# Kernel optimization log

Measured on AMD Instinct MI355X. Metric: run time of the kernel, lower is better.

The kernel has to match this reference:

```python
import jax, jax.numpy as jnp
import numpy as np

B, N, D, S, H = 32, 4096, 256, 16, 512
ITERS = 3
EPS = 1e-8
LN_EPS = 1e-5  # torch LayerNorm default


def _ln(x, w, b):
    m = jnp.mean(x, axis=-1, keepdims=True)
    v = jnp.mean(jnp.square(x - m), axis=-1, keepdims=True)
    return (x - m) / jnp.sqrt(v + LN_EPS) * w + b


def setup_inputs() -> dict:
    key = jax.random.key(0)
    ks = jax.random.split(key, 20)
    s = 1.0 / np.sqrt(D)
    return {
        "inputs": jax.random.normal(ks[0], (B, N, D), jnp.float32),
        "token_weight": jax.random.uniform(ks[1], (B, N), jnp.float32),
        "noise": jax.random.normal(ks[2], (B, S, D), jnp.float32),
        "ln_in_w": jnp.ones((D,), jnp.float32), "ln_in_b": jnp.zeros((D,), jnp.float32),
        "ln_s_w": jnp.ones((D,), jnp.float32), "ln_s_b": jnp.zeros((D,), jnp.float32),
        "ln_m_w": jnp.ones((D,), jnp.float32), "ln_m_b": jnp.zeros((D,), jnp.float32),
        "Wk": jax.random.normal(ks[3], (D, D), jnp.float32) * s,
        "Wv": jax.random.normal(ks[4], (D, D), jnp.float32) * s,
        "Wq": jax.random.normal(ks[5], (D, D), jnp.float32) * s,
        "gru_wih": jax.random.normal(ks[6], (3 * D, D), jnp.float32) * s,
        "gru_whh": jax.random.normal(ks[7], (3 * D, D), jnp.float32) * s,
        "gru_bih": jax.random.normal(ks[8], (3 * D,), jnp.float32) * s,
        "gru_bhh": jax.random.normal(ks[9], (3 * D,), jnp.float32) * s,
        "mlp_w1": jax.random.normal(ks[10], (H, D), jnp.float32) * s,
        "mlp_b1": jnp.zeros((H,), jnp.float32),
        "mlp_w2": jax.random.normal(ks[11], (D, H), jnp.float32) * (1.0 / np.sqrt(H)),
        "mlp_b2": jnp.zeros((D,), jnp.float32),
        "slots_mu": jax.random.normal(ks[12], (1, 1, D), jnp.float32) * 0.02,
        "slots_logsigma": jax.random.normal(ks[13], (1, 1, D), jnp.float32) * 0.02,
    }


def _gru(x, h, wih, whh, bih, bhh):
    # torch GRUCell: gates ordered r, z, n
    gi = x @ wih.T + bih  # [BS, 3D]
    gh = h @ whh.T + bhh
    ir, iz, inn = jnp.split(gi, 3, axis=-1)
    hr, hz, hn = jnp.split(gh, 3, axis=-1)
    r = jax.nn.sigmoid(ir + hr)
    z = jax.nn.sigmoid(iz + hz)
    n = jnp.tanh(inn + r * hn)
    return (1.0 - z) * n + z * h


def reference(inputs, token_weight, noise, ln_in_w, ln_in_b, ln_s_w, ln_s_b,
              ln_m_w, ln_m_b, Wk, Wv, Wq, gru_wih, gru_whh, gru_bih, gru_bhh,
              mlp_w1, mlp_b1, mlp_w2, mlp_b2, slots_mu, slots_logsigma):
    tw = jnp.clip(token_weight, 0.0, None)  # [B,N]
    x = _ln(inputs, ln_in_w, ln_in_b)
    k = x @ Wk.T  # [B,N,D]
    v = x @ Wv.T
    sigma = jnp.clip(jnp.exp(slots_logsigma), 1e-6, None)
    slots = slots_mu + sigma * noise  # [B,S,D]
    scale = D ** (-0.5)
    attn = None
    for _ in range(ITERS):
        slots_prev = slots
        q = _ln(slots, ln_s_w, ln_s_b) @ Wq.T  # [B,S,D]
        logits = jnp.einsum('bnd,bmd->bnm', k, q) * scale  # [B,N,S]
        attn = jax.nn.softmax(logits, axis=-1)  # softmax over slots
        attn = attn * tw[:, :, None]
        attn = attn / (jnp.sum(attn, axis=1, keepdims=True) + EPS)  # normalize over tokens
        updates = jnp.einsum('bnm,bnd->bmd', attn, v)  # [B,S,D]
        slots = _gru(updates.reshape(B * S, D), slots_prev.reshape(B * S, D),
                     gru_wih, gru_whh, gru_bih, gru_bhh).reshape(B, S, D)
        h = jax.nn.gelu(_ln(slots, ln_m_w, ln_m_b) @ mlp_w1.T + mlp_b1, approximate=False)
        slots = slots + h @ mlp_w2.T + mlp_b2
    return slots, attn
```

## Files before the change

kernel.cpp:

```cpp
#include <hip/hip_runtime.h>
#include <hip/hip_bf16.h>
#include <math.h>


#define EPS_ 1e-8f
#define LNEPS_ 1e-5f
#define XSW(r) ((((r)&7)<<3) ^ ((((r)>>3)&3)<<4))
#define GLOAD16(gp, lp) __builtin_amdgcn_global_load_lds( \
    (const __attribute__((address_space(1))) unsigned int*)(gp), \
    (__attribute__((address_space(3))) unsigned int*)(lp), 16, 0, 0)

typedef __attribute__((ext_vector_type(8))) short bf16x8;
typedef __attribute__((ext_vector_type(4))) float f32x4;
typedef __attribute__((ext_vector_type(4))) short s16x4;

static __device__ __forceinline__ short f2bf(float f) {
  __hip_bfloat16 h = __float2bfloat16(f);
  union { __hip_bfloat16 h; short s; } u; u.h = h; return u.s;
}
static __device__ __forceinline__ float4 ld4(const float* p){ return *(const float4*)p; }

__global__ __launch_bounds__(256) void k_prep(
    const float* __restrict__ Wq, const float* __restrict__ Wk,
    const float* __restrict__ wih, const float* __restrict__ Wv,
    const float* __restrict__ whh, const float* __restrict__ w1, const float* __restrict__ w2,
    short* __restrict__ MTb, short* __restrict__ Mb, short* __restrict__ whhb,
    short* __restrict__ w1b, short* __restrict__ w2b) {
  int blk = blockIdx.x, t = threadIdx.x;
  if (blk < 64) {
    int e0 = blk*4;
    float a0=0,a1=0,a2=0,a3=0;
    for (int d=0; d<256; d++) {
      float qv = Wq[d*256 + t];
      a0 += qv*Wk[d*256+e0];   a1 += qv*Wk[d*256+e0+1];
      a2 += qv*Wk[d*256+e0+2]; a3 += qv*Wk[d*256+e0+3];
    }
    MTb[(e0  )*256+t]=f2bf(a0); MTb[(e0+1)*256+t]=f2bf(a1);
    MTb[(e0+2)*256+t]=f2bf(a2); MTb[(e0+3)*256+t]=f2bf(a3);
  } else if (blk < 256) {
    int n0 = (blk-64)*4;
    float a0=0,a1=0,a2=0,a3=0;
    for (int d=0; d<256; d++) {
      float vv = Wv[d*256 + t];
      a0 += wih[(n0  )*256+d]*vv; a1 += wih[(n0+1)*256+d]*vv;
      a2 += wih[(n0+2)*256+d]*vv; a3 += wih[(n0+3)*256+d]*vv;
    }
    Mb[(size_t)(n0  )*256+t]=f2bf(a0); Mb[(size_t)(n0+1)*256+t]=f2bf(a1);
    Mb[(size_t)(n0+2)*256+t]=f2bf(a2); Mb[(size_t)(n0+3)*256+t]=f2bf(a3);
  } else {
    int c = (blk-256)*256 + t;
    const float* src; short* dst;
    if (c < 49152) { src=whh; dst=whhb; }
    else if ((c-=49152) < 32768) { src=w1; dst=w1b; }
    else { c-=32768; src=w2; dst=w2b; }
    float4 v = ld4(src + (size_t)c*4);
    short4 o; o.x=f2bf(v.x); o.y=f2bf(v.y); o.z=f2bf(v.z); o.w=f2bf(v.w);
    *(short4*)(dst + (size_t)c*4) = o;
  }
}

__global__ __launch_bounds__(256) void k3a(
    const float* __restrict__ inputs, const float* __restrict__ lnw, const float* __restrict__ lnb,
    short* __restrict__ xbf, const short* __restrict__ qk, const float* __restrict__ twg,
    float* __restrict__ ux_part, float* __restrict__ colsum_part) {
  __shared__ short Xs[64*264];
  __shared__ short QKs[16*264];
  __shared__ short Pt[16*72];
  __shared__ float tws[64];
  __shared__ float cs[16];
  __shared__ float lnwb[512];
  const int t = threadIdx.x;
  const int b = blockIdx.x >> 4;
  const int n0 = (blockIdx.x & 15) * 256;
  const int lane = t & 63, w = t >> 6, l15 = lane & 15, lg = lane >> 4;
  #pragma unroll
  for (int i=0;i<2;i++){
    int cid = t + i*256;
    int row = cid>>5, ck = cid&31;
    *(uint4*)&QKs[row*264 + ck*8] = *(const uint4*)&qk[((size_t)(b*16+row))*256 + ck*8];
  }
  if (t < 64)       *(float4*)&lnwb[t*4]           = ld4(lnw + t*4);
  else if (t < 128) *(float4*)&lnwb[256+(t-64)*4]  = ld4(lnb + (t-64)*4);
  if (t<16) cs[t]=0.f;
  f32x4 uacc[4] = {};
  for (int g=0; g<4; ++g) {
    __syncthreads();
    const size_t rowbase = (size_t)b*4096 + n0 + g*64;
    {
      const float* ing = inputs + rowbase*256;
      const int r = t>>2, c = t&3;
      float4 vv[16];
      #pragma unroll
      for (int k=0;k<16;k++) vv[k] = ld4(ing + r*256 + (c+4*k)*4);
      float s=0.f, sq=0.f;
      #pragma unroll
      for (int k=0;k<16;k++){
        s  += vv[k].x+vv[k].y+vv[k].z+vv[k].w;
        sq += vv[k].x*vv[k].x+vv[k].y*vv[k].y+vv[k].z*vv[k].z+vv[k].w*vv[k].w;
      }
      s += __shfl_xor(s,1);  s += __shfl_xor(s,2);
      sq += __shfl_xor(sq,1); sq += __shfl_xor(sq,2);
      float mean = s*(1.f/256.f);
      float rstd = rsqrtf(sq*(1.f/256.f) - mean*mean + LNEPS_);
      short* xw = xbf + rowbase*256;
      const int sw = XSW(r);
      #pragma unroll
      for (int k=0;k<16;k++){
        int d0 = (c+4*k)*4;
        float4 wv = *(float4*)&lnwb[d0];
        float4 bv = *(float4*)&lnwb[256+d0];
        s16x4 pk;
        pk[0]=f2bf((vv[k].x-mean)*rstd*wv.x+bv.x);
        pk[1]=f2bf((vv[k].y-mean)*rstd*wv.y+bv.y);
        pk[2]=f2bf((vv[k].z-mean)*rstd*wv.z+bv.z);
        pk[3]=f2bf((vv[k].w-mean)*rstd*wv.w+bv.w);
        *(s16x4*)&Xs[r*264 + d0] = pk;
        *(s16x4*)&xw[r*256 + (d0 ^ sw)] = pk;
      }
    }
    if (t<64) tws[t] = fmaxf(twg[rowbase + t], 0.f);
    __syncthreads();
    f32x4 acc = {0.f,0.f,0.f,0.f};
    #pragma unroll
    for (int kk=0;kk<8;kk++){
      bf16x8 af  = *(const bf16x8*)&Xs[(w*16+l15)*264 + kk*32 + lg*8];
      bf16x8 bfr = *(const bf16x8*)&QKs[l15*264 + kk*32 + lg*8];
      acc = __builtin_amdgcn_mfma_f32_16x16x32_bf16(af, bfr, acc, 0,0,0);
    }
    float a4[4];
    #pragma unroll
    for (int q=0;q<4;q++){
      float v = acc[q]*0.0625f;
      float m = v;
      #pragma unroll
      for (int d=1; d<16; d<<=1) m = fmaxf(m, __shfl_xor(m, d, 16));
      float e = __expf(v-m);
      float se = e;
      #pragma unroll
      for (int d=1; d<16; d<<=1) se += __shfl_xor(se, d, 16);
      int row = w*16 + lg*4 + q;
      a4[q] = (e/se)*tws[row];
    }
    float psum = a4[0]+a4[1]+a4[2]+a4[3];
    psum += __shfl_xor(psum, 16);
    psum += __shfl_xor(psum, 32);
    if (lane<16) atomicAdd(&cs[l15], psum);
    s16x4 pk; pk[0]=f2bf(a4[0]); pk[1]=f2bf(a4[1]); pk[2]=f2bf(a4[2]); pk[3]=f2bf(a4[3]);
    *(s16x4*)&Pt[l15*72 + w*16 + lg*4] = pk;
    __syncthreads();
    #pragma unroll
    for (int kk=0;kk<2;kk++){
      bf16x8 a2 = *(const bf16x8*)&Pt[l15*72 + kk*32 + lg*8];
      #pragma unroll
      for (int tt=0;tt<4;tt++){
        int col = w*64 + tt*16 + l15;
        int rbv = kk*32 + lg*8;
        bf16x8 b2;
        #pragma unroll
        for (int j=0;j<8;j++) b2[j] = Xs[(rbv+j)*264 + col];
        uacc[tt] = __builtin_amdgcn_mfma_f32_16x16x32_bf16(a2, b2, uacc[tt], 0,0,0);
      }
    }
  }
  __syncthreads();
  if (t<16) colsum_part[blockIdx.x*16 + t] = cs[t];
  #pragma unroll
  for (int tt=0;tt<4;tt++){
    #pragma unroll
    for (int q=0;q<4;q++)
      ux_part[(size_t)blockIdx.x*4096 + (lg*4+q)*256 + w*64 + tt*16 + l15] = uacc[tt][q];
  }
}

template<int WATTN>
__global__ __launch_bounds__(256, 2) void k3w(
    const short* __restrict__ xbf, const short* __restrict__ qk,
    const float* __restrict__ twg, float* __restrict__ ux_part,
    float* __restrict__ colsum_part, float* __restrict__ attn_un) {
  __shared__ __align__(16) short XsAll[4][32*256];
  __shared__ __align__(16) short PtAll[4][16*40];
  __shared__ __align__(16) short QKs[16*264];
  __shared__ float csAll[4][16];
  const int t = threadIdx.x;
  const int lane = t & 63, w = t >> 6;
  const int l15 = lane & 15, lg = lane >> 4;
  const int b = blockIdx.x >> 4;
  const size_t wrow0 = (size_t)b*4096 + (blockIdx.x & 15)*256 + w*64;
  short* xs = &XsAll[w][0];
  short* pt = &PtAll[w][0];
  {
    const short* src = xbf + wrow0*256 + lane*8;
    #pragma unroll
    for (int j=0;j<16;j++) GLOAD16(src + j*512, xs + j*512);
  }
  #pragma unroll
  for (int i=0;i<2;i++){
    int cid = t + i*256;
    int row = cid>>5, ck = cid&31;
    *(uint4*)&QKs[row*264 + ck*8] = *(const uint4*)&qk[((size_t)(b*16+row))*256 + ck*8];
  }
  __syncthreads();
  f32x4 acc[16] = {};
  float cs_acc = 0.f;
  for (int tl=0; tl<2; ++tl){
    asm volatile("s_waitcnt vmcnt(0)" ::: "memory");
    const size_t rowb = wrow0 + tl*32;
    #pragma unroll
    for (int sub=0; sub<2; ++sub){
      const int ra = sub*16 + l15, sa = XSW(ra);
      f32x4 a1 = {0.f,0.f,0.f,0.f};
      #pragma unroll
      for (int kk=0;kk<8;kk++){
        bf16x8 af  = *(const bf16x8*)&xs[ra*256 + ((kk*32+lg*8) ^ sa)];
        bf16x8 bfr = *(const bf16x8*)&QKs[l15*264 + kk*32 + lg*8];
        a1 = __builtin_amdgcn_mfma_f32_16x16x32_bf16(af, bfr, a1, 0,0,0);
      }
      float a4[4];
      #pragma unroll
      for (int q=0;q<4;q++){
        float v = a1[q]*0.0625f;
        float m = v;
        #pragma unroll
        for (int d=1; d<16; d<<=1) m = fmaxf(m, __shfl_xor(m, d, 16));
        float e = __expf(v-m);
        float se = e;
        #pragma unroll
        for (int d=1; d<16; d<<=1) se += __shfl_xor(se, d, 16);
        int rloc = sub*16 + lg*4 + q;
        float tw = fmaxf(twg[rowb + rloc], 0.f);
        float a = (e/se)*tw;
        a4[q] = a;
        if (WATTN) attn_un[(rowb + rloc)*16 + l15] = a;
      }
      float psum = a4[0]+a4[1]+a4[2]+a4[3];
      psum += __shfl_xor(psum, 16);
      psum += __shfl_xor(psum, 32);
      cs_acc += psum;
      s16x4 pk; pk[0]=f2bf(a4[0]); pk[1]=f2bf(a4[1]); pk[2]=f2bf(a4[2]); pk[3]=f2bf(a4[3]);
      *(s16x4*)&pt[l15*40 + sub*16 + lg*4] = pk;
    }
    {
      bf16x8 pa = *(const bf16x8*)&pt[l15*40 + lg*8];
      #pragma unroll
      for (int et=0; et<16; ++et){
        bf16x8 b2;
        #pragma unroll
        for (int j=0;j<8;j++){
          int r2 = lg*8 + j;
          b2[j] = xs[r2*256 + ((et*16+l15) ^ XSW(r2))];
        }
        acc[et] = __builtin_amdgcn_mfma_f32_16x16x32_bf16(pa, b2, acc[et], 0,0,0);
      }
    }
    if (tl==0){
      const short* src = xbf + (wrow0+32)*256 + lane*8;
      #pragma unroll
      for (int j=0;j<16;j++) GLOAD16(src + j*512, xs + j*512);
    }
  }
  float* xf = (float*)xs;
  #pragma unroll
  for (int et=0; et<16; ++et)
    #pragma unroll
    for (int q=0;q<4;q++)
      xf[(lg*4+q)*256 + et*16 + l15] = acc[et][q];
  if (lane<16) csAll[w][lane] = cs_acc;
  __syncthreads();
  float* up = ux_part + (size_t)blockIdx.x*4096;
  const float4* X0 = (const float4*)&XsAll[0][0];
  const float4* X1 = (const float4*)&XsAll[1][0];
  const float4* X2 = (const float4*)&XsAll[2][0];
  const float4* X3 = (const float4*)&XsAll[3][0];
  #pragma unroll
  for (int i=0;i<4;i++){
    int idx = t + i*256;
    float4 v0=X0[idx], v1=X1[idx], v2=X2[idx], v3=X3[idx];
    float4 o; o.x=v0.x+v1.x+v2.x+v3.x; o.y=v0.y+v1.y+v2.y+v3.y;
    o.z=v0.z+v1.z+v2.z+v3.z; o.w=v0.w+v1.w+v2.w+v3.w;
    *(float4*)&up[idx*4] = o;
  }
  if (t<16) colsum_part[blockIdx.x*16+t] = csAll[0][t]+csAll[1][t]+csAll[2][t]+csAll[3][t];
}

__global__ __launch_bounds__(256) void k_reduce(const float* __restrict__ uxp,
    const float* __restrict__ csp, short* __restrict__ uxr, float* __restrict__ csr) {
  int r = blockIdx.x;
  int b = r>>4, s = r&15;
  int t = threadIdx.x;
  float cs = 0.f;
  #pragma unroll
  for (int k=0;k<16;k++) cs += csp[((b<<4)+k)*16 + s];
  float u = 0.f;
  #pragma unroll
  for (int k=0;k<16;k++) u += uxp[(size_t)((b<<4)+k)*4096 + s*256 + t];
  uxr[(size_t)r*256+t] = f2bf(u/(cs+EPS_));
  if (t==0) csr[r] = cs;
}

__global__ __launch_bounds__(256) void k_gigh(
    const short* __restrict__ uxr, const short* __restrict__ slotsb,
    const short* __restrict__ Mb, const short* __restrict__ whhb,
    const float* __restrict__ bih, const float* __restrict__ bhh,
    float* __restrict__ gig) {
  __shared__ short As[64*40];
  __shared__ short Ws[64*40];
  const int t=threadIdx.x, bn=blockIdx.x, bm=blockIdx.y;
  const short* A; const short* W; const float* bias; int wo;
  if (bn<12) { A=uxr;    W=Mb   + (size_t)bn*64*256;      bias=bih; wo=bn*64; }
  else       { A=slotsb; W=whhb + (size_t)(bn-12)*64*256; bias=bhh; wo=(bn-12)*64; }
  const int w=t>>6, lane=t&63, l15=lane&15, lg=lane>>4;
  f32x4 acc[4]={};
  for (int k0=0;k0<256;k0+=32){
    __syncthreads();
    *(uint4*)&As[(t>>2)*40+(t&3)*8] = *(const uint4*)&A[(size_t)(bm*64+(t>>2))*256 + k0 + (t&3)*8];
    *(uint4*)&Ws[(t>>2)*40+(t&3)*8] = *(const uint4*)&W[(size_t)(t>>2)*256 + k0 + (t&3)*8];
    __syncthreads();
    bf16x8 af = *(const bf16x8*)&As[(w*16+l15)*40+lg*8];
    #pragma unroll
    for (int ct=0;ct<4;ct++){
      bf16x8 bfr = *(const bf16x8*)&Ws[(ct*16+l15)*40+lg*8];
      acc[ct]=__builtin_amdgcn_mfma_f32_16x16x32_bf16(af,bfr,acc[ct],0,0,0);
    }
  }
  #pragma unroll
  for (int ct=0;ct<4;ct++){
    float bv = bias[wo + ct*16 + l15];
    #pragma unroll
    for (int q=0;q<4;q++){
      int row = bm*64 + w*16 + lg*4 + q;
      gig[(size_t)row*1536 + bn*64 + ct*16 + l15] = acc[ct][q] + bv;
    }
  }
}

__global__ __launch_bounds__(256) void k_mlp1(
    const short* __restrict__ lnmb, const short* __restrict__ w1b,
    const float* __restrict__ b1, short* __restrict__ hb) {
  __shared__ short As[64*40];
  __shared__ short Ws[64*40];
  const int t=threadIdx.x, bn=blockIdx.x, bm=blockIdx.y;
  const int w=t>>6, lane=t&63, l15=lane&15, lg=lane>>4;
  f32x4 acc[4]={};
  for (int k0=0;k0<256;k0+=32){
    __syncthreads();
    *(uint4*)&As[(t>>2)*40+(t&3)*8] = *(const uint4*)&lnmb[(size_t)(bm*64+(t>>2))*256 + k0 + (t&3)*8];
    *(uint4*)&Ws[(t>>2)*40+(t&3)*8] = *(const uint4*)&w1b[(size_t)(bn*64+(t>>2))*256 + k0 + (t&3)*8];
    __syncthreads();
    bf16x8 af = *(const bf16x8*)&As[(w*16+l15)*40+lg*8];
    #pragma unroll
    for (int ct=0;ct<4;ct++){
      bf16x8 bfr = *(const bf16x8*)&Ws[(ct*16+l15)*40+lg*8];
      acc[ct]=__builtin_amdgcn_mfma_f32_16x16x32_bf16(af,bfr,acc[ct],0,0,0);
    }
  }
  #pragma unroll
  for (int ct=0;ct<4;ct++){
    float bv = b1[bn*64 + ct*16 + l15];
    #pragma unroll
    for (int q=0;q<4;q++){
      int row = bm*64 + w*16 + lg*4 + q;
      float v = acc[ct][q] + bv;
      v = 0.5f*v*(1.f+erff(v*0.70710678118654752f));
      hb[(size_t)row*512 + bn*64 + ct*16 + l15] = f2bf(v);
    }
  }
}

__global__ __launch_bounds__(256) void k_gates(const float* __restrict__ gig,
    const float* __restrict__ lw, const float* __restrict__ lb,
    float* __restrict__ slots, short* __restrict__ lnmb) {
  int row  = blockIdx.x*4 + (threadIdx.x>>6);
  int lane = threadIdx.x & 63;
  const float* gi = gig + (size_t)row*1536 + lane*4;
  float4 ir = ld4(gi), iz = ld4(gi+256), inn = ld4(gi+512);
  float4 hr = ld4(gi+768), hz = ld4(gi+1024), hn = ld4(gi+1280);
  float* sp = slots + (size_t)row*256 + lane*4;
  float4 h = ld4(sp);
  float hp[4];
  {
    float r0 = 1.f/(1.f+__expf(-(ir.x+hr.x))); float z0 = 1.f/(1.f+__expf(-(iz.x+hz.x)));
    hp[0] = (1.f-z0)*tanhf(inn.x + r0*hn.x) + z0*h.x;
    float r1 = 1.f/(1.f+__expf(-(ir.y+hr.y))); float z1 = 1.f/(1.f+__expf(-(iz.y+hz.y)));
    hp[1] = (1.f-z1)*tanhf(inn.y + r1*hn.y) + z1*h.y;
    float r2 = 1.f/(1.f+__expf(-(ir.z+hr.z))); float z2 = 1.f/(1.f+__expf(-(iz.z+hz.z)));
    hp[2] = (1.f-z2)*tanhf(inn.z + r2*hn.z) + z2*h.z;
    float r3 = 1.f/(1.f+__expf(-(ir.w+hr.w))); float z3 = 1.f/(1.f+__expf(-(iz.w+hz.w)));
    hp[3] = (1.f-z3)*tanhf(inn.w + r3*hn.w) + z3*h.w;
  }
  float s = hp[0]+hp[1]+hp[2]+hp[3];
  float sq = hp[0]*hp[0]+hp[1]*hp[1]+hp[2]*hp[2]+hp[3]*hp[3];
  #pragma unroll
  for (int d=1; d<64; d<<=1) { s += __shfl_xor(s,d); sq += __shfl_xor(sq,d); }
  float mean = s*(1.f/256.f);
  float rstd = rsqrtf(sq*(1.f/256.f) - mean*mean + LNEPS_);
  float4 wv = ld4(lw+lane*4), bv = ld4(lb+lane*4);
  *(float4*)sp = make_float4(hp[0],hp[1],hp[2],hp[3]);
  short4 o;
  o.x = f2bf((hp[0]-mean)*rstd*wv.x+bv.x);
  o.y = f2bf((hp[1]-mean)*rstd*wv.y+bv.y);
  o.z = f2bf((hp[2]-mean)*rstd*wv.z+bv.z);
  o.w = f2bf((hp[3]-mean)*rstd*wv.w+bv.w);
  *(short4*)(lnmb + (size_t)row*256 + lane*4) = o;
}

template<int MODE>
__global__ __launch_bounds__(256) void k_slotend(
    const short* __restrict__ hb, const short* __restrict__ w2b, const float* __restrict__ b2,
    const float* __restrict__ mu, const float* __restrict__ ls, const float* __restrict__ noise,
    const float* __restrict__ res, float* __restrict__ sout, short* __restrict__ slotsb,
    const float* __restrict__ lnsw, const float* __restrict__ lnsb,
    const short* __restrict__ MTb, short* __restrict__ qk) {
  __shared__ short As[64*40];
  __shared__ short Ws[256*40];
  __shared__ short lnS[64*264];
  const int t=threadIdx.x, bm=blockIdx.x;
  const int w=t>>6, lane=t&63, l15=lane&15, lg=lane>>4;
  float v[16][4];
  if (MODE==1) {
    #pragma unroll
    for (int ct=0;ct<16;ct++){
      int col = ct*16+l15;
      float m = mu[col], sg = fmaxf(__expf(ls[col]),1e-6f);
      #pragma unroll
      for (int q=0;q<4;q++){
        int row = bm*64 + w*16 + lg*4 + q;
        v[ct][q] = m + sg*noise[(size_t)row*256+col];
      }
    }
  } else {
    f32x4 acc[16]={};
    for (int k0=0;k0<512;k0+=32){
      __syncthreads();
      *(uint4*)&As[(t>>2)*40+(t&3)*8] = *(const uint4*)&hb[(size_t)(bm*64+(t>>2))*512 + k0 + (t&3)*8];
      #pragma unroll
      for (int i=0;i<4;i++){ int idx=t+i*256;
        *(uint4*)&Ws[(idx>>2)*40+(idx&3)*8] = *(const uint4*)&w2b[(size_t)(idx>>2)*512 + k0 + (idx&3)*8]; }
      __syncthreads();
      bf16x8 af = *(const bf16x8*)&As[(w*16+l15)*40+lg*8];
      #pragma unroll
      for (int ct=0;ct<16;ct++){
        bf16x8 bfr = *(const bf16x8*)&Ws[(ct*16+l15)*40+lg*8];
        acc[ct]=__builtin_amdgcn_mfma_f32_16x16x32_bf16(af,bfr,acc[ct],0,0,0);
      }
    }
    #pragma unroll
    for (int ct=0;ct<16;ct++){
      int col = ct*16+l15;
      float bv = b2[col];
      #pragma unroll
      for (int q=0;q<4;q++){
        int row = bm*64 + w*16 + lg*4 + q;
        v[ct][q] = acc[ct][q] + bv + res[(size_t)row*256+col];
      }
    }
  }
  float s[4]={0,0,0,0}, sq[4]={0,0,0,0};
  #pragma unroll
  for (int ct=0;ct<16;ct++)
    #pragma unroll
    for (int q=0;q<4;q++){ s[q]+=v[ct][q]; sq[q]+=v[ct][q]*v[ct][q]; }
  #pragma unroll
  for (int q=0;q<4;q++){
    #pragma unroll
    for (int d=1; d<16; d<<=1){ s[q]+=__shfl_xor(s[q],d,16); sq[q]+=__shfl_xor(sq[q],d,16); }
  }
  #pragma unroll
  for (int ct=0;ct<16;ct++){
    int col = ct*16+l15;
    float lw = (MODE!=2) ? lnsw[col] : 0.f;
    float lb = (MODE!=2) ? lnsb[col] : 0.f;
    #pragma unroll
    for (int q=0;q<4;q++){
      int row = bm*64 + w*16 + lg*4 + q;
      sout[(size_t)row*256+col] = v[ct][q];
      if (MODE!=2){
        float mean = s[q]*(1.f/256.f);
        float rstd = rsqrtf(sq[q]*(1.f/256.f)-mean*mean+LNEPS_);
        slotsb[(size_t)row*256+col] = f2bf(v[ct][q]);
        lnS[(w*16+lg*4+q)*264 + col] = f2bf((v[ct][q]-mean)*rstd*lw+lb);
      }
    }
  }
  if (MODE!=2){
    f32x4 qa[16]={};
    for (int k0=0;k0<256;k0+=32){
      __syncthreads();
      #pragma unroll
      for (int i=0;i<4;i++){ int idx=t+i*256;
        *(uint4*)&Ws[(idx>>2)*40+(idx&3)*8] = *(const uint4*)&MTb[(size_t)(idx>>2)*256 + k0 + (idx&3)*8]; }
      __syncthreads();
      bf16x8 af = *(const bf16x8*)&lnS[(w*16+l15)*264 + k0 + lg*8];
      #pragma unroll
      for (int ct=0;ct<16;ct++){
        bf16x8 bfr = *(const bf16x8*)&Ws[(ct*16+l15)*40+lg*8];
        qa[ct]=__builtin_amdgcn_mfma_f32_16x16x32_bf16(af,bfr,qa[ct],0,0,0);
      }
    }
    #pragma unroll
    for (int ct=0;ct<16;ct++)
      #pragma unroll
      for (int q=0;q<4;q++)
        qk[(size_t)(bm*64+w*16+lg*4+q)*256 + ct*16+l15] = f2bf(qa[ct][q]);
  }
}

__global__ __launch_bounds__(256) void k_attn_norm(float* __restrict__ au,
    const float* __restrict__ cs) {
  size_t i = ((size_t)blockIdx.x*256 + threadIdx.x)*4;
  float4 v = ld4(au + i);
  int s = (int)(i & 15);
  size_t b = i >> 16;
  const float* c = cs + b*16 + s;
  float4 o;
  o.x = v.x/(c[0]+EPS_); o.y = v.y/(c[1]+EPS_);
  o.z = v.z/(c[2]+EPS_); o.w = v.w/(c[3]+EPS_);
  *(float4*)(au + i) = o;
}

extern "C" void kernel_launch(void* const* d_in, const int* in_sizes, int n_in,
                              void* d_out, int out_size, void* d_ws, size_t ws_size,
                              hipStream_t stream) {
  const float* inputs   = (const float*)d_in[0];
  const float* token_w  = (const float*)d_in[1];
  const float* noise    = (const float*)d_in[2];
  const float* ln_in_w  = (const float*)d_in[3];
  const float* ln_in_b  = (const float*)d_in[4];
  const float* ln_s_w   = (const float*)d_in[5];
  const float* ln_s_b   = (const float*)d_in[6];
  const float* ln_m_w   = (const float*)d_in[7];
  const float* ln_m_b   = (const float*)d_in[8];
  const float* Wk       = (const float*)d_in[9];
  const float* Wv       = (const float*)d_in[10];
  const float* Wq       = (const float*)d_in[11];
  const float* gru_wih  = (const float*)d_in[12];
  const float* gru_whh  = (const float*)d_in[13];
  const float* gru_bih  = (const float*)d_in[14];
  const float* gru_bhh  = (const float*)d_in[15];
  const float* mlp_w1   = (const float*)d_in[16];
  const float* mlp_b1   = (const float*)d_in[17];
  const float* mlp_w2   = (const float*)d_in[18];
  const float* mlp_b2   = (const float*)d_in[19];
  const float* slots_mu = (const float*)d_in[20];
  const float* slots_ls = (const float*)d_in[21];

  float* out_slots = (float*)d_out;
  float* out_attn  = out_slots + 131072;

  char* wsb = (char*)d_ws;
  size_t off = 0;
  short* xbf     = (short*)(wsb + off); off += 67108864;
  float* ux_part = (float*)(wsb + off); off += 8388608;
  float* cs_part = (float*)(wsb + off); off += 32768;
  float* cs_red  = (float*)(wsb + off); off += 2048;
  short* qk      = (short*)(wsb + off); off += 262144;
  short* uxr     = (short*)(wsb + off); off += 262144;
  short* MTb     = (short*)(wsb + off); off += 131072;
  short* Mb      = (short*)(wsb + off); off += 393216;
  float* gig     = (float*)(wsb + off); off += 3145728;
  float* slots   = (float*)(wsb + off); off += 524288;
  short* slotsb  = (short*)(wsb + off); off += 262144;
  short* lnmb    = (short*)(wsb + off); off += 262144;
  short* hb      = (short*)(wsb + off); off += 524288;
  short* whhb    = (short*)(wsb + off); off += 393216;
  short* w1b     = (short*)(wsb + off); off += 262144;
  short* w2b     = (short*)(wsb + off); off += 262144;

  k_prep<<<704,256,0,stream>>>(Wq, Wk, gru_wih, Wv, gru_whh, mlp_w1, mlp_w2,
                               MTb, Mb, whhb, w1b, w2b);
  k_slotend<1><<<8,256,0,stream>>>(nullptr, nullptr, nullptr, slots_mu, slots_ls, noise,
                                   nullptr, slots, slotsb, ln_s_w, ln_s_b, MTb, qk);
  for (int it=0; it<3; ++it) {
    if (it==0)
      k3a<<<512,256,0,stream>>>(inputs, ln_in_w, ln_in_b, xbf, qk, token_w,
                                ux_part, cs_part);
    else if (it==1)
      k3w<0><<<512,256,0,stream>>>(xbf, qk, token_w, ux_part, cs_part, out_attn);
    else
      k3w<1><<<512,256,0,stream>>>(xbf, qk, token_w, ux_part, cs_part, out_attn);
    k_reduce<<<512,256,0,stream>>>(ux_part, cs_part, uxr, cs_red);
    k_gigh<<<dim3(24,8),256,0,stream>>>(uxr, slotsb, Mb, whhb, gru_bih, gru_bhh, gig);
    k_gates<<<128,256,0,stream>>>(gig, ln_m_w, ln_m_b, slots, lnmb);
    k_mlp1<<<dim3(8,8),256,0,stream>>>(lnmb, w1b, mlp_b1, hb);
    if (it<2)
      k_slotend<0><<<8,256,0,stream>>>(hb, w2b, mlp_b2, nullptr, nullptr, nullptr,
                                       slots, slots, slotsb, ln_s_w, ln_s_b, MTb, qk);
    else
      k_slotend<2><<<8,256,0,stream>>>(hb, w2b, mlp_b2, nullptr, nullptr, nullptr,
                                       slots, out_slots, slotsb, ln_s_w, ln_s_b, MTb, qk);
  }
  k_attn_norm<<<2048,256,0,stream>>>(out_attn, cs_red);
}
```

Measured before the change: 250.2 us.

## Restructure attention kernel into block-cooperative double-buffered 64-row groups

The per-wave attention/update kernel, where each wave owned 64 rows and produced full 16x256 partial updates, is replaced by a block-cooperative version. The block streams its 256 rows in four 64-row groups through a double-buffered LDS tile, prefetching the next group while computing the current one. Each wave now owns a 64-column slice of the update accumulator, which removes the final cross-wave LDS reduction and cuts accumulator registers from 16 tiles to 4. Token weights are staged in LDS and column sums use shared atomics. In exchange it adds block barriers per group and drops the two-blocks-per-CU launch bound hint.

Measured after the change: 241.4 us. 3.5% less time.

```diff
diff --git a/kernel.cpp b/kernel.cpp
--- a/kernel.cpp
+++ b/kernel.cpp
@@ -173,113 +173,106 @@
 }
 
 template<int WATTN>
-__global__ __launch_bounds__(256, 2) void k3w(
+__global__ __launch_bounds__(256) void k3b(
     const short* __restrict__ xbf, const short* __restrict__ qk,
     const float* __restrict__ twg, float* __restrict__ ux_part,
     float* __restrict__ colsum_part, float* __restrict__ attn_un) {
-  __shared__ __align__(16) short XsAll[4][32*256];
-  __shared__ __align__(16) short PtAll[4][16*40];
+  __shared__ __align__(16) short Xd[2][64*256];
+  __shared__ __align__(16) short Pt[2][16*72];
   __shared__ __align__(16) short QKs[16*264];
-  __shared__ float csAll[4][16];
+  __shared__ float tws_all[256];
+  __shared__ float cs[16];
   const int t = threadIdx.x;
-  const int lane = t & 63, w = t >> 6;
-  const int l15 = lane & 15, lg = lane >> 4;
+  const int lane = t & 63, w = t >> 6, l15 = lane & 15, lg = lane >> 4;
   const int b = blockIdx.x >> 4;
-  const size_t wrow0 = (size_t)b*4096 + (blockIdx.x & 15)*256 + w*64;
-  short* xs = &XsAll[w][0];
-  short* pt = &PtAll[w][0];
-  {
-    const short* src = xbf + wrow0*256 + lane*8;
-    #pragma unroll
-    for (int j=0;j<16;j++) GLOAD16(src + j*512, xs + j*512);
-  }
+  const int n0 = (blockIdx.x & 15) * 256;
+  const size_t base = (size_t)b*4096 + n0;
+#define DMA_GROUP(buf, g) do { \
+    const short* _src = xbf + (base + (size_t)(g)*64 + w*16)*256 + lane*8; \
+    short* _dst = &Xd[buf][(w*16)*256]; \
+    _Pragma("unroll") \
+    for (int _j=0;_j<8;_j++) GLOAD16(_src + _j*512, _dst + _j*512); \
+  } while(0)
+  DMA_GROUP(0, 0);
   #pragma unroll
   for (int i=0;i<2;i++){
     int cid = t + i*256;
     int row = cid>>5, ck = cid&31;
     *(uint4*)&QKs[row*264 + ck*8] = *(const uint4*)&qk[((size_t)(b*16+row))*256 + ck*8];
   }
+  tws_all[t] = fmaxf(twg[base + t], 0.f);
+  if (t<16) cs[t]=0.f;
   __syncthreads();
-  f32x4 acc[16] = {};
-  float cs_acc = 0.f;
-  for (int tl=0; tl<2; ++tl){
-    asm volatile("s_waitcnt vmcnt(0)" ::: "memory");
-    const size_t rowb = wrow0 + tl*32;
-    #pragma unroll
-    for (int sub=0; sub<2; ++sub){
-      const int ra = sub*16 + l15, sa = XSW(ra);
-      f32x4 a1 = {0.f,0.f,0.f,0.f};
+  f32x4 uacc[4] = {};
+  for (int g=0; g<4; ++g) {
+    short* xs = &Xd[g&1][0];
+    short* pt = &Pt[g&1][0];
+    if (g<3){
+      DMA_GROUP((g+1)&1, g+1);
+      asm volatile("s_waitcnt vmcnt(8)" ::: "memory");
+    } else {
+      asm volatile("s_waitcnt vmcnt(0)" ::: "memory");
+    }
+    f32x4 acc = {0.f,0.f,0.f,0.f};
+    {
+      const int ra = w*16 + l15, sa = XSW(ra);
       #pragma unroll
       for (int kk=0;kk<8;kk++){
         bf16x8 af  = *(const bf16x8*)&xs[ra*256 + ((kk*32+lg*8) ^ sa)];
         bf16x8 bfr = *(const bf16x8*)&QKs[l15*264 + kk*32 + lg*8];
-        a1 = __builtin_amdgcn_mfma_f32_16x16x32_bf16(af, bfr, a1, 0,0,0);
-      }
-      float a4[4];
-      #pragma unroll
-      for (int q=0;q<4;q++){
-        float v = a1[q]*0.0625f;
-        float m = v;
-        #pragma unroll
-        for (int d=1; d<16; d<<=1) m = fmaxf(m, __shfl_xor(m, d, 16));
-        float e = __expf(v-m);
-        float se = e;
-        #pragma unroll
-        for (int d=1; d<16; d<<=1) se += __shfl_xor(se, d, 16);
-        int rloc = sub*16 + lg*4 + q;
-        float tw = fmaxf(twg[rowb + rloc], 0.f);
-        float a = (e/se)*tw;
-        a4[q] = a;
-        if (WATTN) attn_un[(rowb + rloc)*16 + l15] = a;
-      }
-      float psum = a4[0]+a4[1]+a4[2]+a4[3];
-      psum += __shfl_xor(psum, 16);
-      psum += __shfl_xor(psum, 32);
-      cs_acc += psum;
-      s16x4 pk; pk[0]=f2bf(a4[0]); pk[1]=f2bf(a4[1]); pk[2]=f2bf(a4[2]); pk[3]=f2bf(a4[3]);
-      *(s16x4*)&pt[l15*40 + sub*16 + lg*4] = pk;
-    }
-    {
-      bf16x8 pa = *(const bf16x8*)&pt[l15*40 + lg*8];
-      #pragma unroll
-      for (int et=0; et<16; ++et){
+        acc = __builtin_amdgcn_mfma_f32_16x16x32_bf16(af, bfr, acc, 0,0,0);
+      }
+    }
+    float a4[4];
+    #pragma unroll
+    for (int q=0;q<4;q++){
+      float v = acc[q]*0.0625f;
+      float m = v;
+      #pragma unroll
+      for (int d=1; d<16; d<<=1) m = fmaxf(m, __shfl_xor(m, d, 16));
+      float e = __expf(v-m);
+      float se = e;
+      #pragma unroll
+      for (int d=1; d<16; d<<=1) se += __shfl_xor(se, d, 16);
+      int rloc = w*16 + lg*4 + q;
+      float a = (e/se)*tws_all[g*64 + rloc];
+      a4[q] = a;
+      if (WATTN) attn_un[(base + g*64 + rloc)*16 + l15] = a;
+    }
+    float psum = a4[0]+a4[1]+a4[2]+a4[3];
+    psum += __shfl_xor(psum, 16);
+    psum += __shfl_xor(psum, 32);
+    if (lane<16) atomicAdd(&cs[l15], psum);
+    s16x4 pk; pk[0]=f2bf(a4[0]); pk[1]=f2bf(a4[1]); pk[2]=f2bf(a4[2]); pk[3]=f2bf(a4[3]);
+    *(s16x4*)&pt[l15*72 + w*16 + lg*4] = pk;
+    asm volatile("s_waitcnt lgkmcnt(0)" ::: "memory");
+    __builtin_amdgcn_s_barrier();
+    #pragma unroll
+    for (int kk=0;kk<2;kk++){
+      bf16x8 a2 = *(const bf16x8*)&pt[l15*72 + kk*32 + lg*8];
+      #pragma unroll
+      for (int tt=0;tt<4;tt++){
+        int col = w*64 + tt*16 + l15;
         bf16x8 b2;
         #pragma unroll
         for (int j=0;j<8;j++){
-          int r2 = lg*8 + j;
-          b2[j] = xs[r2*256 + ((et*16+l15) ^ XSW(r2))];
+          int r2 = kk*32 + lg*8 + j;
+          b2[j] = xs[r2*256 + (col ^ XSW(r2))];
         }
-        acc[et] = __builtin_amdgcn_mfma_f32_16x16x32_bf16(pa, b2, acc[et], 0,0,0);
-      }
-    }
-    if (tl==0){
-      const short* src = xbf + (wrow0+32)*256 + lane*8;
-      #pragma unroll
-      for (int j=0;j<16;j++) GLOAD16(src + j*512, xs + j*512);
-    }
-  }
-  float* xf = (float*)xs;
-  #pragma unroll
-  for (int et=0; et<16; ++et)
+        uacc[tt] = __builtin_amdgcn_mfma_f32_16x16x32_bf16(a2, b2, uacc[tt], 0,0,0);
+      }
+    }
+    asm volatile("s_waitcnt lgkmcnt(0)" ::: "memory");
+    __builtin_amdgcn_s_barrier();
+  }
+  if (t<16) colsum_part[blockIdx.x*16 + t] = cs[t];
+  #pragma unroll
+  for (int tt=0;tt<4;tt++){
     #pragma unroll
     for (int q=0;q<4;q++)
-      xf[(lg*4+q)*256 + et*16 + l15] = acc[et][q];
-  if (lane<16) csAll[w][lane] = cs_acc;
-  __syncthreads();
-  float* up = ux_part + (size_t)blockIdx.x*4096;
-  const float4* X0 = (const float4*)&XsAll[0][0];
-  const float4* X1 = (const float4*)&XsAll[1][0];
-  const float4* X2 = (const float4*)&XsAll[2][0];
-  const float4* X3 = (const float4*)&XsAll[3][0];
-  #pragma unroll
-  for (int i=0;i<4;i++){
-    int idx = t + i*256;
-    float4 v0=X0[idx], v1=X1[idx], v2=X2[idx], v3=X3[idx];
-    float4 o; o.x=v0.x+v1.x+v2.x+v3.x; o.y=v0.y+v1.y+v2.y+v3.y;
-    o.z=v0.z+v1.z+v2.z+v3.z; o.w=v0.w+v1.w+v2.w+v3.w;
-    *(float4*)&up[idx*4] = o;
-  }
-  if (t<16) colsum_part[blockIdx.x*16+t] = csAll[0][t]+csAll[1][t]+csAll[2][t]+csAll[3][t];
+      ux_part[(size_t)blockIdx.x*4096 + (lg*4+q)*256 + w*64 + tt*16 + l15] = uacc[tt][q];
+  }
+#undef DMA_GROUP
 }
 
 __global__ __launch_bounds__(256) void k_reduce(const float* __restrict__ uxp,
@@ -574,9 +567,9 @@
       k3a<<<512,256,0,stream>>>(inputs, ln_in_w, ln_in_b, xbf, qk, token_w,
                                 ux_part, cs_part);
     else if (it==1)
-      k3w<0><<<512,256,0,stream>>>(xbf, qk, token_w, ux_part, cs_part, out_attn);
+      k3b<0><<<512,256,0,stream>>>(xbf, qk, token_w, ux_part, cs_part, out_attn);
     else
-      k3w<1><<<512,256,0,stream>>>(xbf, qk, token_w, ux_part, cs_part, out_attn);
+      k3b<1><<<512,256,0,stream>>>(xbf, qk, token_w, ux_part, cs_part, out_attn);
     k_reduce<<<512,256,0,stream>>>(ux_part, cs_part, uxr, cs_red);
     k_gigh<<<dim3(24,8),256,0,stream>>>(uxr, slotsb, Mb, whhb, gru_bih, gru_bhh, gig);
     k_gates<<<128,256,0,stream>>>(gig, ln_m_w, ln_m_b, slots, lnmb);
```

## Split attention-iteration kernel into logits/softmax and update-GEMM kernels

Applied to the files above, without the earlier changes.

For iterations 2 and 3, the fused k3w kernel is replaced by two kernels. k3A computes logits and softmax over 2048 small blocks and writes the bf16 attention tiles to global memory. k3B reloads x and computes attn^T·v partials, storing them in bf16 instead of fp32. The aim is more parallelism and less partial-sum traffic, at the cost of reading the 64MB xbf twice per iteration plus an extra launch. Partial sums are rounded to bf16 before the reduction, which adds some precision loss.

After: 268.3 us. 1.07x slower.

```diff
diff --git a/kernel.cpp b/kernel.cpp
--- a/kernel.cpp
+++ b/kernel.cpp
@@ -17,6 +17,9 @@
 static __device__ __forceinline__ short f2bf(float f) {
   __hip_bfloat16 h = __float2bfloat16(f);
   union { __hip_bfloat16 h; short s; } u; u.h = h; return u.s;
+}
+static __device__ __forceinline__ float bf2f(short s) {
+  union { float f; unsigned u; } x; x.u = ((unsigned)(unsigned short)s) << 16; return x.f;
 }
 static __device__ __forceinline__ float4 ld4(const float* p){ return *(const float4*)p; }
 
@@ -173,25 +176,22 @@
 }
 
 template<int WATTN>
-__global__ __launch_bounds__(256, 2) void k3w(
+__global__ __launch_bounds__(256) void k3A(
     const short* __restrict__ xbf, const short* __restrict__ qk,
-    const float* __restrict__ twg, float* __restrict__ ux_part,
+    const float* __restrict__ twg, short* __restrict__ Pg,
     float* __restrict__ colsum_part, float* __restrict__ attn_un) {
-  __shared__ __align__(16) short XsAll[4][32*256];
-  __shared__ __align__(16) short PtAll[4][16*40];
+  __shared__ __align__(16) short XsAll[4][16*256];
   __shared__ __align__(16) short QKs[16*264];
-  __shared__ float csAll[4][16];
+  __shared__ float cs[16];
   const int t = threadIdx.x;
-  const int lane = t & 63, w = t >> 6;
-  const int l15 = lane & 15, lg = lane >> 4;
-  const int b = blockIdx.x >> 4;
-  const size_t wrow0 = (size_t)b*4096 + (blockIdx.x & 15)*256 + w*64;
+  const int lane = t & 63, w = t >> 6, l15 = lane & 15, lg = lane >> 4;
+  const int b = blockIdx.x >> 6;
+  const size_t grow0 = (size_t)b*4096 + (blockIdx.x & 63)*64 + w*16;
   short* xs = &XsAll[w][0];
-  short* pt = &PtAll[w][0];
   {
-    const short* src = xbf + wrow0*256 + lane*8;
-    #pragma unroll
-    for (int j=0;j<16;j++) GLOAD16(src + j*512, xs + j*512);
+    const short* src = xbf + grow0*256 + lane*8;
+    #pragma unroll
+    for (int j=0;j<8;j++) GLOAD16(src + j*512, xs + j*512);
   }
   #pragma unroll
   for (int i=0;i<2;i++){
@@ -199,100 +199,115 @@
     int row = cid>>5, ck = cid&31;
     *(uint4*)&QKs[row*264 + ck*8] = *(const uint4*)&qk[((size_t)(b*16+row))*256 + ck*8];
   }
+  if (t<16) cs[t]=0.f;
   __syncthreads();
+  f32x4 acc = {0.f,0.f,0.f,0.f};
+  {
+    const int sa = XSW((w&1)*16 + l15);
+    #pragma unroll
+    for (int kk=0;kk<8;kk++){
+      bf16x8 af  = *(const bf16x8*)&xs[l15*256 + ((kk*32+lg*8) ^ sa)];
+      bf16x8 bfr = *(const bf16x8*)&QKs[l15*264 + kk*32 + lg*8];
+      acc = __builtin_amdgcn_mfma_f32_16x16x32_bf16(af, bfr, acc, 0,0,0);
+    }
+  }
+  float a4[4];
+  #pragma unroll
+  for (int q=0;q<4;q++){
+    float v = acc[q]*0.0625f;
+    float m = v;
+    #pragma unroll
+    for (int d=1; d<16; d<<=1) m = fmaxf(m, __shfl_xor(m, d, 16));
+    float e = __expf(v-m);
+    float se = e;
+    #pragma unroll
+    for (int d=1; d<16; d<<=1) se += __shfl_xor(se, d, 16);
+    int rloc = lg*4 + q;
+    float tw = fmaxf(twg[grow0 + rloc], 0.f);
+    float a = (e/se)*tw;
+    a4[q] = a;
+    if (WATTN) attn_un[(grow0 + rloc)*16 + l15] = a;
+  }
+  float psum = a4[0]+a4[1]+a4[2]+a4[3];
+  psum += __shfl_xor(psum, 16);
+  psum += __shfl_xor(psum, 32);
+  if (lane<16) atomicAdd(&cs[l15], psum);
+  s16x4 pk; pk[0]=f2bf(a4[0]); pk[1]=f2bf(a4[1]); pk[2]=f2bf(a4[2]); pk[3]=f2bf(a4[3]);
+  *(s16x4*)&Pg[(size_t)(blockIdx.x*4 + w)*256 + l15*16 + lg*4] = pk;
+  __syncthreads();
+  if (t<16) colsum_part[blockIdx.x*16 + t] = cs[t];
+}
+
+__global__ __launch_bounds__(256) void k3B(
+    const short* __restrict__ xbf, const short* __restrict__ Pg,
+    short* __restrict__ ux_part) {
+  __shared__ __align__(16) short XsAll[4][32*256];
+  const int t = threadIdx.x;
+  const int lane = t & 63, w = t >> 6, l15 = lane & 15, lg = lane >> 4;
+  const int tile = blockIdx.x*4 + w;
+  const size_t grow0 = (size_t)tile*32;
+  short* xs = &XsAll[w][0];
+  {
+    const short* src = xbf + grow0*256 + lane*8;
+    #pragma unroll
+    for (int j=0;j<16;j++) GLOAD16(src + j*512, xs + j*512);
+  }
+  bf16x8 pa = *(const bf16x8*)&Pg[(size_t)(tile*2 + (lg>>1))*256 + l15*16 + (lg&1)*8];
+  asm volatile("s_waitcnt vmcnt(0)" ::: "memory");
   f32x4 acc[16] = {};
-  float cs_acc = 0.f;
-  for (int tl=0; tl<2; ++tl){
-    asm volatile("s_waitcnt vmcnt(0)" ::: "memory");
-    const size_t rowb = wrow0 + tl*32;
-    #pragma unroll
-    for (int sub=0; sub<2; ++sub){
-      const int ra = sub*16 + l15, sa = XSW(ra);
-      f32x4 a1 = {0.f,0.f,0.f,0.f};
-      #pragma unroll
-      for (int kk=0;kk<8;kk++){
-        bf16x8 af  = *(const bf16x8*)&xs[ra*256 + ((kk*32+lg*8) ^ sa)];
-        bf16x8 bfr = *(const bf16x8*)&QKs[l15*264 + kk*32 + lg*8];
-        a1 = __builtin_amdgcn_mfma_f32_16x16x32_bf16(af, bfr, a1, 0,0,0);
-      }
-      float a4[4];
-      #pragma unroll
-      for (int q=0;q<4;q++){
-        float v = a1[q]*0.0625f;
-        float m = v;
-        #pragma unroll
-        for (int d=1; d<16; d<<=1) m = fmaxf(m, __shfl_xor(m, d, 16));
-        float e = __expf(v-m);
-        float se = e;
-        #pragma unroll
-        for (int d=1; d<16; d<<=1) se += __shfl_xor(se, d, 16);
-        int rloc = sub*16 + lg*4 + q;
-        float tw = fmaxf(twg[rowb + rloc], 0.f);
-        float a = (e/se)*tw;
-        a4[q] = a;
-        if (WATTN) attn_un[(rowb + rloc)*16 + l15] = a;
-      }
-      float psum = a4[0]+a4[1]+a4[2]+a4[3];
-      psum += __shfl_xor(psum, 16);
-      psum += __shfl_xor(psum, 32);
-      cs_acc += psum;
-      s16x4 pk; pk[0]=f2bf(a4[0]); pk[1]=f2bf(a4[1]); pk[2]=f2bf(a4[2]); pk[3]=f2bf(a4[3]);
-      *(s16x4*)&pt[l15*40 + sub*16 + lg*4] = pk;
-    }
-    {
-      bf16x8 pa = *(const bf16x8*)&pt[l15*40 + lg*8];
-      #pragma unroll
-      for (int et=0; et<16; ++et){
-        bf16x8 b2;
-        #pragma unroll
-        for (int j=0;j<8;j++){
-          int r2 = lg*8 + j;
-          b2[j] = xs[r2*256 + ((et*16+l15) ^ XSW(r2))];
-        }
-        acc[et] = __builtin_amdgcn_mfma_f32_16x16x32_bf16(pa, b2, acc[et], 0,0,0);
-      }
-    }
-    if (tl==0){
-      const short* src = xbf + (wrow0+32)*256 + lane*8;
-      #pragma unroll
-      for (int j=0;j<16;j++) GLOAD16(src + j*512, xs + j*512);
-    }
-  }
-  float* xf = (float*)xs;
-  #pragma unroll
-  for (int et=0; et<16; ++et)
+  #pragma unroll
+  for (int et=0; et<16; ++et){
+    bf16x8 b2;
+    #pragma unroll
+    for (int j=0;j<8;j++){
+      int r2 = lg*8 + j;
+      b2[j] = xs[r2*256 + ((et*16+l15) ^ XSW(r2))];
+    }
+    acc[et] = __builtin_amdgcn_mfma_f32_16x16x32_bf16(pa, b2, acc[et], 0,0,0);
+  }
+  #pragma unroll
+  for (int et=0;et<16;et++)
     #pragma unroll
     for (int q=0;q<4;q++)
-      xf[(lg*4+q)*256 + et*16 + l15] = acc[et][q];
-  if (lane<16) csAll[w][lane] = cs_acc;
+      xs[(lg*4+q)*256 + et*16 + l15] = f2bf(acc[et][q]);
   __syncthreads();
-  float* up = ux_part + (size_t)blockIdx.x*4096;
-  const float4* X0 = (const float4*)&XsAll[0][0];
-  const float4* X1 = (const float4*)&XsAll[1][0];
-  const float4* X2 = (const float4*)&XsAll[2][0];
-  const float4* X3 = (const float4*)&XsAll[3][0];
-  #pragma unroll
-  for (int i=0;i<4;i++){
+  short* up = ux_part + (size_t)blockIdx.x*4096;
+  #pragma unroll
+  for (int i=0;i<2;i++){
     int idx = t + i*256;
-    float4 v0=X0[idx], v1=X1[idx], v2=X2[idx], v3=X3[idx];
-    float4 o; o.x=v0.x+v1.x+v2.x+v3.x; o.y=v0.y+v1.y+v2.y+v3.y;
-    o.z=v0.z+v1.z+v2.z+v3.z; o.w=v0.w+v1.w+v2.w+v3.w;
-    *(float4*)&up[idx*4] = o;
-  }
-  if (t<16) colsum_part[blockIdx.x*16+t] = csAll[0][t]+csAll[1][t]+csAll[2][t]+csAll[3][t];
-}
-
-__global__ __launch_bounds__(256) void k_reduce(const float* __restrict__ uxp,
+    uint4 v0 = *(const uint4*)&XsAll[0][idx*8];
+    uint4 v1 = *(const uint4*)&XsAll[1][idx*8];
+    uint4 v2 = *(const uint4*)&XsAll[2][idx*8];
+    uint4 v3 = *(const uint4*)&XsAll[3][idx*8];
+    const short* s0=(const short*)&v0; const short* s1=(const short*)&v1;
+    const short* s2=(const short*)&v2; const short* s3=(const short*)&v3;
+    short o[8];
+    #pragma unroll
+    for (int j=0;j<8;j++)
+      o[j] = f2bf(bf2f(s0[j])+bf2f(s1[j])+bf2f(s2[j])+bf2f(s3[j]));
+    *(uint4*)&up[idx*8] = *(const uint4*)o;
+  }
+}
+
+template<int UXCH, int CSCH, int UXBF>
+__global__ __launch_bounds__(256) void k_reduceT(const void* __restrict__ uxp,
     const float* __restrict__ csp, short* __restrict__ uxr, float* __restrict__ csr) {
   int r = blockIdx.x;
   int b = r>>4, s = r&15;
   int t = threadIdx.x;
   float cs = 0.f;
-  #pragma unroll
-  for (int k=0;k<16;k++) cs += csp[((b<<4)+k)*16 + s];
+  #pragma unroll 8
+  for (int k=0;k<CSCH;k++) cs += csp[(b*CSCH+k)*16 + s];
   float u = 0.f;
-  #pragma unroll
-  for (int k=0;k<16;k++) u += uxp[(size_t)((b<<4)+k)*4096 + s*256 + t];
+  if (UXBF) {
+    const short* p = (const short*)uxp;
+    #pragma unroll 8
+    for (int k=0;k<UXCH;k++) u += bf2f(p[(size_t)(b*UXCH+k)*4096 + s*256 + t]);
+  } else {
+    const float* p = (const float*)uxp;
+    #pragma unroll 8
+    for (int k=0;k<UXCH;k++) u += p[(size_t)(b*UXCH+k)*4096 + s*256 + t];
+  }
   uxr[(size_t)r*256+t] = f2bf(u/(cs+EPS_));
   if (t==0) csr[r] = cs;
 }
@@ -549,8 +564,11 @@
   char* wsb = (char*)d_ws;
   size_t off = 0;
   short* xbf     = (short*)(wsb + off); off += 67108864;
-  float* ux_part = (float*)(wsb + off); off += 8388608;
-  float* cs_part = (float*)(wsb + off); off += 32768;
+  float* ux_p0   = (float*)(wsb + off); off += 8388608;
+  float* cs_p0   = (float*)(wsb + off); off += 32768;
+  short* ux_pB   = (short*)(wsb + off); off += 8388608;
+  float* cs_pA   = (float*)(wsb + off); off += 131072;
+  short* Pg      = (short*)(wsb + off); off += 4194304;
   float* cs_red  = (float*)(wsb + off); off += 2048;
   short* qk      = (short*)(wsb + off); off += 262144;
   short* uxr     = (short*)(wsb + off); off += 262144;
@@ -570,14 +588,18 @@
   k_slotend<1><<<8,256,0,stream>>>(nullptr, nullptr, nullptr, slots_mu, slots_ls, noise,
                                    nullptr, slots, slotsb, ln_s_w, ln_s_b, MTb, qk);
   for (int it=0; it<3; ++it) {
-    if (it==0)
+    if (it==0) {
       k3a<<<512,256,0,stream>>>(inputs, ln_in_w, ln_in_b, xbf, qk, token_w,
-                                ux_part, cs_part);
-    else if (it==1)
-      k3w<0><<<512,256,0,stream>>>(xbf, qk, token_w, ux_part, cs_part, out_attn);
-    else
-      k3w<1><<<512,256,0,stream>>>(xbf, qk, token_w, ux_part, cs_part, out_attn);
-    k_reduce<<<512,256,0,stream>>>(ux_part, cs_part, uxr, cs_red);
+                                ux_p0, cs_p0);
+      k_reduceT<16,16,0><<<512,256,0,stream>>>(ux_p0, cs_p0, uxr, cs_red);
+    } else {
+      if (it==1)
+        k3A<0><<<2048,256,0,stream>>>(xbf, qk, token_w, Pg, cs_pA, out_attn);
+      else
+        k3A<1><<<2048,256,0,stream>>>(xbf, qk, token_w, Pg, cs_pA, out_attn);
+      k3B<<<1024,256,0,stream>>>(xbf, Pg, ux_pB);
+      k_reduceT<32,64,1><<<512,256,0,stream>>>(ux_pB, cs_pA, uxr, cs_red);
+    }
     k_gigh<<<dim3(24,8),256,0,stream>>>(uxr, slotsb, Mb, whhb, gru_bih, gru_bhh, gig);
     k_gates<<<128,256,0,stream>>>(gig, ln_m_w, ln_m_b, slots, lnmb);
     k_mlp1<<<dim3(8,8),256,0,stream>>>(lnmb, w1b, mlp_b1, hb);
```
